# Optimization experiments

Measured on AMD Instinct MI355X. Metric: run time of the kernel, lower is better.

The kernel has to match this reference:

```python
import jax, jax.numpy as jnp
import numpy as np

N, E = 50000, 300000
IN_C, HID, OUT_C, HEADS = 256, 64, 128, 4
HW = HID * HEADS  # 256


def gat_conv(x, edge_index, W, att_src, att_dst, bias, concat):
    # x: [N, F_in], W: [F_in, H*C], att_*: [H, C], edge_index: [2, E] (src -> dst)
    H, C = att_src.shape
    n = x.shape[0]
    src, dst = edge_index[0], edge_index[1]
    h = (x @ W).reshape(n, H, C)                      # [N, H, C]
    a_src = jnp.einsum('nhc,hc->nh', h, att_src)      # [N, H]
    a_dst = jnp.einsum('nhc,hc->nh', h, att_dst)      # [N, H]
    e = jax.nn.leaky_relu(a_src[src] + a_dst[dst], 0.2)  # [E, H]
    m = jax.ops.segment_max(e, dst, num_segments=n)   # per-dst max for stable softmax
    m = jnp.where(jnp.isfinite(m), m, 0.0)
    ex = jnp.exp(e - m[dst])                          # [E, H]
    denom = jax.ops.segment_sum(ex, dst, num_segments=n)
    alpha = ex / (denom[dst] + 1e-16)                 # [E, H]
    msg = h[src] * alpha[:, :, None]                  # [E, H, C]
    out = jax.ops.segment_sum(msg, dst, num_segments=n)  # [N, H, C]
    if concat:
        return out.reshape(n, H * C) + bias
    return out.mean(axis=1) + bias


def setup_inputs() -> dict:
    key = jax.random.key(0)
    ks = jax.random.split(key, 24)
    inp = {}
    inp['x'] = jax.random.normal(ks[0], (N, IN_C), dtype=jnp.float32)
    inp['edge_index'] = jax.random.randint(ks[1], (2, E), 0, N, dtype=jnp.int32)
    def glorot(k, shape):
        fan = shape[0] + shape[-1]
        return jax.random.uniform(k, shape, jnp.float32, -1.0, 1.0) * np.sqrt(6.0 / fan)
    # layer 0: GATConv(256 -> 64, heads=4, concat) + Linear(256 -> 256)
    inp['W0'] = glorot(ks[2], (IN_C, HW)); inp['as0'] = glorot(ks[3], (HEADS, HID)); inp['ad0'] = glorot(ks[4], (HEADS, HID)); inp['b0'] = jnp.zeros((HW,), jnp.float32)
    inp['lw0'] = glorot(ks[5], (IN_C, HW)); inp['lb0'] = jnp.zeros((HW,), jnp.float32)
    # layer 1: GATConv(256 -> 64, heads=4, concat) + Linear(256 -> 256)
    inp['W1'] = glorot(ks[6], (HW, HW)); inp['as1'] = glorot(ks[7], (HEADS, HID)); inp['ad1'] = glorot(ks[8], (HEADS, HID)); inp['b1'] = jnp.zeros((HW,), jnp.float32)
    inp['lw1'] = glorot(ks[9], (HW, HW)); inp['lb1'] = jnp.zeros((HW,), jnp.float32)
    # layer 2: GATConv(256 -> 128, heads=4, concat=False mean) + Linear(256 -> 128)
    inp['W2'] = glorot(ks[10], (HW, HEADS * OUT_C)); inp['as2'] = glorot(ks[11], (HEADS, OUT_C)); inp['ad2'] = glorot(ks[12], (HEADS, OUT_C)); inp['b2'] = jnp.zeros((OUT_C,), jnp.float32)
    inp['lw2'] = glorot(ks[13], (HW, OUT_C)); inp['lb2'] = jnp.zeros((OUT_C,), jnp.float32)
    return inp


def reference(x, edge_index, W0, as0, ad0, b0, lw0, lb0, W1, as1, ad1, b1, lw1, lb1, W2, as2, ad2, b2, lw2, lb2):
    # layer 0
    h = gat_conv(x, edge_index, W0, as0, ad0, b0, concat=True) + (x @ lw0 + lb0)
    h = jax.nn.elu(h)  # dropout p=0.0 -> identity
    # layer 1
    h = gat_conv(h, edge_index, W1, as1, ad1, b1, concat=True) + (h @ lw1 + lb1)
    h = jax.nn.elu(h)
    # layer 2 (no activation)
    out = gat_conv(h, edge_index, W2, as2, ad2, b2, concat=False) + (h @ lw2 + lb2)
    return out
```

## Files before the change

### kernel.cpp

```cpp
#include <hip/hip_runtime.h>
#include <cstddef>


typedef __bf16 bf16x8 __attribute__((ext_vector_type(8)));
typedef float floatx4 __attribute__((ext_vector_type(4)));

__device__ __forceinline__ unsigned short bf16_rn(float f) {
    unsigned int u = __float_as_uint(f);
    u += 0x7FFF + ((u >> 16) & 1);
    return (unsigned short)(u >> 16);
}
__device__ __forceinline__ float bf16_tof(unsigned short h) {
    return __uint_as_float(((unsigned int)h) << 16);
}


__global__ void degree_kernel(const int* __restrict__ dst, int* __restrict__ deg, int E) {
    int e = blockIdx.x * 256 + threadIdx.x;
    if (e < E) atomicAdd(&deg[dst[e]], 1);
}

__global__ __launch_bounds__(1024) void scan_kernel(const int* __restrict__ deg,
                                                    int* __restrict__ off, int n) {
    __shared__ int wsum[16];
    __shared__ int carry_s;
    int tid = threadIdx.x, lane = tid & 63, wid = tid >> 6;
    if (tid == 0) { carry_s = 0; off[0] = 0; }
    __syncthreads();
    for (int base = 0; base < n; base += 1024) {
        int i = base + tid;
        int v = (i < n) ? deg[i] : 0;
        int s = v;
        #pragma unroll
        for (int d = 1; d < 64; d <<= 1) {
            int t = __shfl_up(s, d, 64);
            if (lane >= d) s += t;
        }
        if (lane == 63) wsum[wid] = s;
        __syncthreads();
        if (wid == 0) {
            int wv = (lane < 16) ? wsum[lane] : 0;
            #pragma unroll
            for (int d = 1; d < 16; d <<= 1) {
                int t = __shfl_up(wv, d, 64);
                if (lane >= d) wv += t;
            }
            if (lane < 16) wsum[lane] = wv;
        }
        __syncthreads();
        int prev = (wid > 0) ? wsum[wid - 1] : 0;
        int inc = carry_s + prev + s;
        if (i < n) off[i + 1] = inc;
        int chunk_total = wsum[15];
        __syncthreads();
        if (tid == 0) carry_s += chunk_total;
        __syncthreads();
    }
}

__global__ void scatter_kernel(const int* __restrict__ src, const int* __restrict__ dst,
                               const int* __restrict__ off, int* __restrict__ cursor,
                               int* __restrict__ csrc, int E) {
    int e = blockIdx.x * 256 + threadIdx.x;
    if (e < E) {
        int d = dst[e];
        int p = off[d] + atomicAdd(&cursor[d], 1);
        csrc[p] = src[e];
    }
}


__global__ __launch_bounds__(256) void wprep_kernel(
    const float* __restrict__ W0, const float* __restrict__ lw0,
    const float* __restrict__ W1, const float* __restrict__ lw1,
    const float* __restrict__ W2, const float* __restrict__ lw2,
    ushort* __restrict__ B0h, ushort* __restrict__ B0l,
    ushort* __restrict__ B1h, ushort* __restrict__ B1l,
    ushort* __restrict__ B2h, ushort* __restrict__ B2l,
    const float* __restrict__ as0, const float* __restrict__ ad0,
    const float* __restrict__ as1, const float* __restrict__ ad1,
    const float* __restrict__ as2, const float* __restrict__ ad2,
    float* __restrict__ vsd0, float* __restrict__ vsd1, float* __restrict__ vsd2)
{
    int bid = blockIdx.x, tid = threadIdx.x;
    if (bid < 1664) {
        const float* src; ushort* dh; ushort* dl; int Ncols, roff, base;
        if (bid < 256)       { src = W0;  dh = B0h; dl = B0l; Ncols = 256; roff = 0;   base = 0; }
        else if (bid < 512)  { src = lw0; dh = B0h; dl = B0l; Ncols = 256; roff = 256; base = 256; }
        else if (bid < 768)  { src = W1;  dh = B1h; dl = B1l; Ncols = 256; roff = 0;   base = 512; }
        else if (bid < 1024) { src = lw1; dh = B1h; dl = B1l; Ncols = 256; roff = 256; base = 768; }
        else if (bid < 1536) { src = W2;  dh = B2h; dl = B2l; Ncols = 512; roff = 0;   base = 1024; }
        else                 { src = lw2; dh = B2h; dl = B2l; Ncols = 128; roff = 512; base = 1536; }
        int idx = (bid - base) * 256 + tid;
        int k = idx / Ncols, n = idx - k * Ncols;
        float v = src[idx];
        unsigned short hi = bf16_rn(v);
        unsigned short lo = bf16_rn(v - bf16_tof(hi));
        int row = n + roff;
        int poff = ((row >> 4) * 8 + (k >> 5)) * 512 + (((row & 15) + 16 * ((k & 31) >> 3)) << 3) + (k & 7);
        dh[poff] = hi;
        dl[poff] = lo;
    } else {
        int fj = (bid - 1664) >> 2;
        int idx = ((bid - 1664) & 3) * 256 + tid;
        const float *W, *as_, *ad_; float* vsd; int C;
        if (fj == 0)      { W = W0; as_ = as0; ad_ = ad0; vsd = vsd0; C = 64; }
        else if (fj == 1) { W = W1; as_ = as1; ad_ = ad1; vsd = vsd1; C = 64; }
        else              { W = W2; as_ = as2; ad_ = ad2; vsd = vsd2; C = 128; }
        int k = idx >> 2, hh = idx & 3;
        const float* wp = W + (size_t)k * (4 * C) + hh * C;
        float s = 0.f, d = 0.f;
        for (int c = 0; c < C; c++) {
            float w = wp[c];
            s += w * as_[hh * C + c];
            d += w * ad_[hh * C + c];
        }
        vsd[k * 8 + hh] = s;
        vsd[k * 8 + 4 + hh] = d;
    }
}


__global__ __launch_bounds__(256) void split_att_kernel(
    const float* __restrict__ x, const float* __restrict__ vsd,
    ushort* __restrict__ Aph, ushort* __restrict__ Apl,
    float* __restrict__ asrc, float* __restrict__ adst, int n)
{
    int wid = threadIdx.x >> 6, lane = threadIdx.x & 63;
    int d = blockIdx.x * 4 + wid;
    if (d >= n) return;
    int k0 = lane * 4;
    float4 v = *(const float4*)(x + (size_t)d * 256 + k0);
    ushort4 hi, lo;
    hi.x = bf16_rn(v.x); lo.x = bf16_rn(v.x - bf16_tof(hi.x));
    hi.y = bf16_rn(v.y); lo.y = bf16_rn(v.y - bf16_tof(hi.y));
    hi.z = bf16_rn(v.z); lo.z = bf16_rn(v.z - bf16_tof(hi.z));
    hi.w = bf16_rn(v.w); lo.w = bf16_rn(v.w - bf16_tof(hi.w));
    int poff = ((d >> 4) * 8 + (k0 >> 5)) * 512 + (((d & 15) + 16 * ((k0 & 31) >> 3)) << 3) + (k0 & 7);
    *(ushort4*)(Aph + poff) = hi;
    *(ushort4*)(Apl + poff) = lo;

    const float* vp = vsd + (size_t)k0 * 8;
    float4 r0a = *(const float4*)(vp + 0),  r0b = *(const float4*)(vp + 4);
    float4 r1a = *(const float4*)(vp + 8),  r1b = *(const float4*)(vp + 12);
    float4 r2a = *(const float4*)(vp + 16), r2b = *(const float4*)(vp + 20);
    float4 r3a = *(const float4*)(vp + 24), r3b = *(const float4*)(vp + 28);
    float4 pa, pb;
    pa.x = v.x * r0a.x + v.y * r1a.x + v.z * r2a.x + v.w * r3a.x;
    pa.y = v.x * r0a.y + v.y * r1a.y + v.z * r2a.y + v.w * r3a.y;
    pa.z = v.x * r0a.z + v.y * r1a.z + v.z * r2a.z + v.w * r3a.z;
    pa.w = v.x * r0a.w + v.y * r1a.w + v.z * r2a.w + v.w * r3a.w;
    pb.x = v.x * r0b.x + v.y * r1b.x + v.z * r2b.x + v.w * r3b.x;
    pb.y = v.x * r0b.y + v.y * r1b.y + v.z * r2b.y + v.w * r3b.y;
    pb.z = v.x * r0b.z + v.y * r1b.z + v.z * r2b.z + v.w * r3b.z;
    pb.w = v.x * r0b.w + v.y * r1b.w + v.z * r2b.w + v.w * r3b.w;
    #pragma unroll
    for (int o = 1; o < 64; o <<= 1) {
        pa.x += __shfl_xor(pa.x, o, 64); pa.y += __shfl_xor(pa.y, o, 64);
        pa.z += __shfl_xor(pa.z, o, 64); pa.w += __shfl_xor(pa.w, o, 64);
        pb.x += __shfl_xor(pb.x, o, 64); pb.y += __shfl_xor(pb.y, o, 64);
        pb.z += __shfl_xor(pb.z, o, 64); pb.w += __shfl_xor(pb.w, o, 64);
    }
    if (lane == 0) {
        *(float4*)(asrc + (size_t)d * 4) = pa;
        *(float4*)(adst + (size_t)d * 4) = pb;
    }
}

__global__ __launch_bounds__(256) void amax_kernel(const float* __restrict__ asrc,
                                                   unsigned int* __restrict__ amax, int n) {
    int tid = threadIdx.x;
    float4 m4 = make_float4(-1e30f, -1e30f, -1e30f, -1e30f);
    for (int i = blockIdx.x * 256 + tid; i < n; i += gridDim.x * 256) {
        float4 v = ((const float4*)asrc)[i];
        m4.x = fmaxf(m4.x, v.x); m4.y = fmaxf(m4.y, v.y);
        m4.z = fmaxf(m4.z, v.z); m4.w = fmaxf(m4.w, v.w);
    }
    #pragma unroll
    for (int o = 32; o > 0; o >>= 1) {
        m4.x = fmaxf(m4.x, __shfl_down(m4.x, o, 64));
        m4.y = fmaxf(m4.y, __shfl_down(m4.y, o, 64));
        m4.z = fmaxf(m4.z, __shfl_down(m4.z, o, 64));
        m4.w = fmaxf(m4.w, __shfl_down(m4.w, o, 64));
    }
    __shared__ float sm[4][4];
    int wid = tid >> 6, lane = tid & 63;
    if (lane == 0) { sm[wid][0] = m4.x; sm[wid][1] = m4.y; sm[wid][2] = m4.z; sm[wid][3] = m4.w; }
    __syncthreads();
    if (tid < 4) {
        float v = fmaxf(fmaxf(sm[0][tid], sm[1][tid]), fmaxf(sm[2][tid], sm[3][tid]));
        unsigned int u = __float_as_uint(v);
        u = (u >> 31) ? ~u : (u | 0x80000000u);
        atomicMax(&amax[tid], u);
    }
}

__device__ __forceinline__ float amax_decode(unsigned int u) {
    unsigned int bits = (u >> 31) ? (u & 0x7FFFFFFFu) : ~u;
    return __uint_as_float(bits);
}


__global__ __launch_bounds__(256, 2) void gemm_mfma_kernel(
    const ushort* __restrict__ Aph, const ushort* __restrict__ Apl,
    const ushort* __restrict__ Bph, const ushort* __restrict__ Bpl,
    ushort* __restrict__ O1, int n1, ushort* __restrict__ O2,
    const float* __restrict__ bias2,
    int gm, int M, int N)
{
    int gy = N >> 7;
    int bid = blockIdx.x;
    int k8 = bid & 7, sb = bid >> 3;
    int ny = sb % gy, bxi = sb / gy;
    int bx = bxi * 8 + k8;
    if (bx >= gm) return;
    int bm = bx * 128, bn = ny * 128;

    int tid = threadIdx.x, lane = tid & 63, wv = tid >> 6;
    int wm = (wv >> 1) * 64, wn = (wv & 1) * 64;
    int fr = lane & 15, q = lane >> 4;

    size_t aoff = (size_t)((bm + wm) >> 4) * 4096 + lane * 8;
    size_t boff = (size_t)((bn + wn) >> 4) * 4096 + lane * 8;

    floatx4 acc[4][4] = {};
    bf16x8 cah[4], cal[4], cbh[4], cbl[4];
    bf16x8 nah[4], nal[4], nbh[4], nbl[4];

    #pragma unroll
    for (int i = 0; i < 4; ++i) {
        cah[i] = *(const bf16x8*)(Aph + aoff + i * 4096);
        cal[i] = *(const bf16x8*)(Apl + aoff + i * 4096);
        cbh[i] = *(const bf16x8*)(Bph + boff + i * 4096);
        cbl[i] = *(const bf16x8*)(Bpl + boff + i * 4096);
    }

    #pragma unroll
    for (int it = 0; it < 8; ++it) {
        if (it < 7) {
            int co = (it + 1) * 512;
            #pragma unroll
            for (int i = 0; i < 4; ++i) {
                nah[i] = *(const bf16x8*)(Aph + aoff + i * 4096 + co);
                nal[i] = *(const bf16x8*)(Apl + aoff + i * 4096 + co);
                nbh[i] = *(const bf16x8*)(Bph + boff + i * 4096 + co);
                nbl[i] = *(const bf16x8*)(Bpl + boff + i * 4096 + co);
            }
        }
        #pragma unroll
        for (int i = 0; i < 4; ++i)
            #pragma unroll
            for (int j = 0; j < 4; ++j) {
                acc[i][j] = __builtin_amdgcn_mfma_f32_16x16x32_bf16(cah[i], cbh[j], acc[i][j], 0, 0, 0);
                acc[i][j] = __builtin_amdgcn_mfma_f32_16x16x32_bf16(cah[i], cbl[j], acc[i][j], 0, 0, 0);
                acc[i][j] = __builtin_amdgcn_mfma_f32_16x16x32_bf16(cal[i], cbh[j], acc[i][j], 0, 0, 0);
            }
        if (it < 7) {
            #pragma unroll
            for (int i = 0; i < 4; ++i) {
                cah[i] = nah[i]; cal[i] = nal[i];
                cbh[i] = nbh[i]; cbl[i] = nbl[i];
            }
        }
    }

    int n2 = N - n1;
    #pragma unroll
    for (int i = 0; i < 4; ++i) {
        #pragma unroll
        for (int r = 0; r < 4; ++r) {
            int grow = bm + wm + i * 16 + q * 4 + r;
            if (grow < M) {
                #pragma unroll
                for (int j = 0; j < 4; ++j) {
                    int gcol = bn + wn + j * 16 + fr;
                    float v = acc[i][j][r];
                    if (gcol < n1) {
                        O1[(size_t)grow * n1 + gcol] = bf16_rn(v);
                    } else {
                        v += bias2[gcol - n1];
                        O2[(size_t)grow * n2 + (gcol - n1)] = bf16_rn(v);
                    }
                }
            }
        }
    }
}


__global__ __launch_bounds__(256, 8) void agg01_kernel(
    const ushort* __restrict__ h,
    const float* __restrict__ asrc, const float* __restrict__ adst,
    const unsigned int* __restrict__ amax,
    const int* __restrict__ off, const int* __restrict__ csrc,
    const ushort* __restrict__ lin,
    const float* __restrict__ bias,
    ushort* __restrict__ Aph, ushort* __restrict__ Apl,
    const float* __restrict__ vsd_next,
    float* __restrict__ asrc_out, float* __restrict__ adst_out,
    int n)
{
    int wid = threadIdx.x >> 6, lane = threadIdx.x & 63;
    int d = blockIdx.x * 4 + wid;
    if (d >= n) return;
    int head = lane >> 4;
    int c0 = lane * 4;
    float a_d = adst[d * 4 + head];
    float mh = amax_decode(amax[head]) + a_d;
    float m = (mh > 0.f) ? mh : 0.2f * mh;
    int s0 = off[d], s1 = off[d + 1];

    float denom = 0.f, a0 = 0.f, a1 = 0.f, a2 = 0.f, a3 = 0.f;
    int i = s0;
    for (; i + 4 <= s1; i += 4) {
        int sa = csrc[i], sb = csrc[i + 1], sc = csrc[i + 2], sd = csrc[i + 3];
        float ea = asrc[sa * 4 + head];
        float eb = asrc[sb * 4 + head];
        float ec = asrc[sc * 4 + head];
        float ed = asrc[sd * 4 + head];
        ushort4 hva = *(const ushort4*)(h + (size_t)sa * 256 + c0);
        ushort4 hvb = *(const ushort4*)(h + (size_t)sb * 256 + c0);
        ushort4 hvc = *(const ushort4*)(h + (size_t)sc * 256 + c0);
        ushort4 hvd = *(const ushort4*)(h + (size_t)sd * 256 + c0);
        ea += a_d; ea = (ea > 0.f) ? ea : 0.2f * ea; float wa = __expf(ea - m);
        eb += a_d; eb = (eb > 0.f) ? eb : 0.2f * eb; float wb = __expf(eb - m);
        ec += a_d; ec = (ec > 0.f) ? ec : 0.2f * ec; float wc = __expf(ec - m);
        ed += a_d; ed = (ed > 0.f) ? ed : 0.2f * ed; float wd = __expf(ed - m);
        denom += wa;
        a0 += wa * bf16_tof(hva.x); a1 += wa * bf16_tof(hva.y);
        a2 += wa * bf16_tof(hva.z); a3 += wa * bf16_tof(hva.w);
        denom += wb;
        a0 += wb * bf16_tof(hvb.x); a1 += wb * bf16_tof(hvb.y);
        a2 += wb * bf16_tof(hvb.z); a3 += wb * bf16_tof(hvb.w);
        denom += wc;
        a0 += wc * bf16_tof(hvc.x); a1 += wc * bf16_tof(hvc.y);
        a2 += wc * bf16_tof(hvc.z); a3 += wc * bf16_tof(hvc.w);
        denom += wd;
        a0 += wd * bf16_tof(hvd.x); a1 += wd * bf16_tof(hvd.y);
        a2 += wd * bf16_tof(hvd.z); a3 += wd * bf16_tof(hvd.w);
    }
    for (; i < s1; ++i) {
        int s = csrc[i];
        float e = asrc[s * 4 + head] + a_d;
        e = (e > 0.f) ? e : 0.2f * e;
        float w = __expf(e - m);
        denom += w;
        ushort4 hv = *(const ushort4*)(h + (size_t)s * 256 + c0);
        a0 += w * bf16_tof(hv.x);
        a1 += w * bf16_tof(hv.y);
        a2 += w * bf16_tof(hv.z);
        a3 += w * bf16_tof(hv.w);
    }
    float inv = 1.f / (denom + 1e-16f);
    float4 b4 = *(const float4*)(bias + c0);
    ushort4 l4 = *(const ushort4*)(lin + (size_t)d * 256 + c0);
    float v0 = a0 * inv + b4.x + bf16_tof(l4.x);
    float v1 = a1 * inv + b4.y + bf16_tof(l4.y);
    float v2 = a2 * inv + b4.z + bf16_tof(l4.z);
    float v3 = a3 * inv + b4.w + bf16_tof(l4.w);
    v0 = (v0 > 0.f) ? v0 : (__expf(v0) - 1.f);
    v1 = (v1 > 0.f) ? v1 : (__expf(v1) - 1.f);
    v2 = (v2 > 0.f) ? v2 : (__expf(v2) - 1.f);
    v3 = (v3 > 0.f) ? v3 : (__expf(v3) - 1.f);

    ushort4 oh, ol;
    oh.x = bf16_rn(v0); ol.x = bf16_rn(v0 - bf16_tof(oh.x));
    oh.y = bf16_rn(v1); ol.y = bf16_rn(v1 - bf16_tof(oh.y));
    oh.z = bf16_rn(v2); ol.z = bf16_rn(v2 - bf16_tof(oh.z));
    oh.w = bf16_rn(v3); ol.w = bf16_rn(v3 - bf16_tof(oh.w));
    int poff = ((d >> 4) * 8 + (c0 >> 5)) * 512 + (((d & 15) + 16 * ((c0 & 31) >> 3)) << 3) + (c0 & 7);
    *(ushort4*)(Aph + poff) = oh;
    *(ushort4*)(Apl + poff) = ol;

    const float* vp = vsd_next + (size_t)c0 * 8;
    float4 r0a = *(const float4*)(vp + 0),  r0b = *(const float4*)(vp + 4);
    float4 r1a = *(const float4*)(vp + 8),  r1b = *(const float4*)(vp + 12);
    float4 r2a = *(const float4*)(vp + 16), r2b = *(const float4*)(vp + 20);
    float4 r3a = *(const float4*)(vp + 24), r3b = *(const float4*)(vp + 28);
    float4 pa, pb;
    pa.x = v0 * r0a.x + v1 * r1a.x + v2 * r2a.x + v3 * r3a.x;
    pa.y = v0 * r0a.y + v1 * r1a.y + v2 * r2a.y + v3 * r3a.y;
    pa.z = v0 * r0a.z + v1 * r1a.z + v2 * r2a.z + v3 * r3a.z;
    pa.w = v0 * r0a.w + v1 * r1a.w + v2 * r2a.w + v3 * r3a.w;
    pb.x = v0 * r0b.x + v1 * r1b.x + v2 * r2b.x + v3 * r3b.x;
    pb.y = v0 * r0b.y + v1 * r1b.y + v2 * r2b.y + v3 * r3b.y;
    pb.z = v0 * r0b.z + v1 * r1b.z + v2 * r2b.z + v3 * r3b.z;
    pb.w = v0 * r0b.w + v1 * r1b.w + v2 * r2b.w + v3 * r3b.w;
    #pragma unroll
    for (int o = 1; o < 64; o <<= 1) {
        pa.x += __shfl_xor(pa.x, o, 64); pa.y += __shfl_xor(pa.y, o, 64);
        pa.z += __shfl_xor(pa.z, o, 64); pa.w += __shfl_xor(pa.w, o, 64);
        pb.x += __shfl_xor(pb.x, o, 64); pb.y += __shfl_xor(pb.y, o, 64);
        pb.z += __shfl_xor(pb.z, o, 64); pb.w += __shfl_xor(pb.w, o, 64);
    }
    if (lane == 0) {
        *(float4*)(asrc_out + (size_t)d * 4) = pa;
        *(float4*)(adst_out + (size_t)d * 4) = pb;
    }
}


__global__ __launch_bounds__(256, 8) void agg2_kernel(
    const ushort* __restrict__ h,
    const float* __restrict__ asrc, const float* __restrict__ adst,
    const unsigned int* __restrict__ amax,
    const int* __restrict__ off, const int* __restrict__ csrc,
    const ushort* __restrict__ lin,
    const float* __restrict__ bias,
    float* __restrict__ out,
    int n)
{
    int wid = threadIdx.x >> 6, lane = threadIdx.x & 63;
    int d = blockIdx.x * 4 + wid;
    if (d >= n) return;
    int ha = lane >> 5;
    int hb = ha + 2;
    int c0 = lane * 4;
    float ad_a = adst[d * 4 + ha];
    float ad_b = adst[d * 4 + hb];
    float mha = amax_decode(amax[ha]) + ad_a;
    float mhb = amax_decode(amax[hb]) + ad_b;
    float ma = (mha > 0.f) ? mha : 0.2f * mha;
    float mb = (mhb > 0.f) ? mhb : 0.2f * mhb;
    int s0 = off[d], s1 = off[d + 1];

    float da = 0.f, db = 0.f;
    floatx4 aa = {0.f, 0.f, 0.f, 0.f}, ab = {0.f, 0.f, 0.f, 0.f};
    int i = s0;
    for (; i + 2 <= s1; i += 2) {
        int sx = csrc[i], sy = csrc[i + 1];
        float eax = asrc[sx * 4 + ha];
        float ebx = asrc[sx * 4 + hb];
        float eay = asrc[sy * 4 + ha];
        float eby = asrc[sy * 4 + hb];
        ushort4 vax = *(const ushort4*)(h + (size_t)sx * 512 + c0);
        ushort4 vbx = *(const ushort4*)(h + (size_t)sx * 512 + 256 + c0);
        ushort4 vay = *(const ushort4*)(h + (size_t)sy * 512 + c0);
        ushort4 vby = *(const ushort4*)(h + (size_t)sy * 512 + 256 + c0);
        eax += ad_a; eax = (eax > 0.f) ? eax : 0.2f * eax; float wax = __expf(eax - ma);
        ebx += ad_b; ebx = (ebx > 0.f) ? ebx : 0.2f * ebx; float wbx = __expf(ebx - mb);
        eay += ad_a; eay = (eay > 0.f) ? eay : 0.2f * eay; float way = __expf(eay - ma);
        eby += ad_b; eby = (eby > 0.f) ? eby : 0.2f * eby; float wby = __expf(eby - mb);
        da += wax; db += wbx;
        aa[0] += wax * bf16_tof(vax.x); aa[1] += wax * bf16_tof(vax.y);
        aa[2] += wax * bf16_tof(vax.z); aa[3] += wax * bf16_tof(vax.w);
        ab[0] += wbx * bf16_tof(vbx.x); ab[1] += wbx * bf16_tof(vbx.y);
        ab[2] += wbx * bf16_tof(vbx.z); ab[3] += wbx * bf16_tof(vbx.w);
        da += way; db += wby;
        aa[0] += way * bf16_tof(vay.x); aa[1] += way * bf16_tof(vay.y);
        aa[2] += way * bf16_tof(vay.z); aa[3] += way * bf16_tof(vay.w);
        ab[0] += wby * bf16_tof(vby.x); ab[1] += wby * bf16_tof(vby.y);
        ab[2] += wby * bf16_tof(vby.z); ab[3] += wby * bf16_tof(vby.w);
    }
    for (; i < s1; ++i) {
        int s = csrc[i];
        float ea = asrc[s * 4 + ha] + ad_a;
        float eb = asrc[s * 4 + hb] + ad_b;
        ea = (ea > 0.f) ? ea : 0.2f * ea;
        eb = (eb > 0.f) ? eb : 0.2f * eb;
        float wa = __expf(ea - ma), wb = __expf(eb - mb);
        da += wa; db += wb;
        ushort4 va = *(const ushort4*)(h + (size_t)s * 512 + c0);
        ushort4 vb = *(const ushort4*)(h + (size_t)s * 512 + 256 + c0);
        aa[0] += wa * bf16_tof(va.x); aa[1] += wa * bf16_tof(va.y);
        aa[2] += wa * bf16_tof(va.z); aa[3] += wa * bf16_tof(va.w);
        ab[0] += wb * bf16_tof(vb.x); ab[1] += wb * bf16_tof(vb.y);
        ab[2] += wb * bf16_tof(vb.z); ab[3] += wb * bf16_tof(vb.w);
    }
    float ia = 1.f / (da + 1e-16f), ib = 1.f / (db + 1e-16f);
    float s4[4];
    #pragma unroll
    for (int j = 0; j < 4; ++j) s4[j] = aa[j] * ia + ab[j] * ib;
    float p4[4];
    #pragma unroll
    for (int j = 0; j < 4; ++j) p4[j] = __shfl_xor(s4[j], 32, 64);
    if (lane < 32) {
        float4 b4 = *(const float4*)(bias + c0);
        ushort4 l4 = *(const ushort4*)(lin + (size_t)d * 128 + c0);
        float4 o;
        o.x = 0.25f * (s4[0] + p4[0]) + b4.x + bf16_tof(l4.x);
        o.y = 0.25f * (s4[1] + p4[1]) + b4.y + bf16_tof(l4.y);
        o.z = 0.25f * (s4[2] + p4[2]) + b4.z + bf16_tof(l4.z);
        o.w = 0.25f * (s4[3] + p4[3]) + b4.w + bf16_tof(l4.w);
        *(float4*)(out + (size_t)d * 128 + c0) = o;
    }
}


extern "C" void kernel_launch(void* const* d_in, const int* in_sizes, int n_in,
                              void* d_out, int out_size, void* d_ws, size_t ws_size,
                              hipStream_t stream)
{
    const float* x   = (const float*)d_in[0];
    const int*   ei  = (const int*)d_in[1];
    const float* W0  = (const float*)d_in[2];
    const float* as0 = (const float*)d_in[3];
    const float* ad0 = (const float*)d_in[4];
    const float* b0  = (const float*)d_in[5];
    const float* lw0 = (const float*)d_in[6];
    const float* lb0 = (const float*)d_in[7];
    const float* W1  = (const float*)d_in[8];
    const float* as1 = (const float*)d_in[9];
    const float* ad1 = (const float*)d_in[10];
    const float* b1  = (const float*)d_in[11];
    const float* lw1 = (const float*)d_in[12];
    const float* lb1 = (const float*)d_in[13];
    const float* W2  = (const float*)d_in[14];
    const float* as2 = (const float*)d_in[15];
    const float* ad2 = (const float*)d_in[16];
    const float* b2  = (const float*)d_in[17];
    const float* lw2 = (const float*)d_in[18];
    const float* lb2 = (const float*)d_in[19];
    float* out = (float*)d_out;

    const int N = in_sizes[0] / 256;
    const int E = in_sizes[1] / 2;
    const int* esrc = ei;
    const int* edst = ei + E;

    const int gm = (N + 127) / 128;
    const int gmp = ((gm + 7) / 8) * 8;
    const size_t Agroups = (size_t)gm * 8;

    char* p = (char*)d_ws;
    ushort* act_hi = (ushort*)p; p += Agroups * 8 * 512 * 2;
    ushort* act_lo = (ushort*)p; p += Agroups * 8 * 512 * 2;
    ushort* h      = (ushort*)p; p += (size_t)N * 512 * 2;
    ushort* lin    = (ushort*)p; p += (size_t)N * 256 * 2;
    float*  as_a   = (float*)p;  p += (size_t)N * 4 * 4;
    float*  ad_a   = (float*)p;  p += (size_t)N * 4 * 4;
    float*  as_b   = (float*)p;  p += (size_t)N * 4 * 4;
    float*  ad_b   = (float*)p;  p += (size_t)N * 4 * 4;
    ushort* B0h = (ushort*)p; p += (size_t)32 * 8 * 512 * 2;
    ushort* B0l = (ushort*)p; p += (size_t)32 * 8 * 512 * 2;
    ushort* B1h = (ushort*)p; p += (size_t)32 * 8 * 512 * 2;
    ushort* B1l = (ushort*)p; p += (size_t)32 * 8 * 512 * 2;
    ushort* B2h = (ushort*)p; p += (size_t)40 * 8 * 512 * 2;
    ushort* B2l = (ushort*)p; p += (size_t)40 * 8 * 512 * 2;
    float* vsd0 = (float*)p; p += 256 * 8 * 4;
    float* vsd1 = (float*)p; p += 256 * 8 * 4;
    float* vsd2 = (float*)p; p += 256 * 8 * 4;
    unsigned int* amax = (unsigned int*)p;
    int* deg    = (int*)(amax + 12);
    int* off    = deg + N;
    int* cursor = off + N + 1;
    int* csrc   = cursor + N;

    hipMemsetAsync(amax, 0, sizeof(int) * (size_t)(3 * N + 13), stream);

    int egrid = (E + 255) / 256;
    degree_kernel<<<egrid, 256, 0, stream>>>(edst, deg, E);
    scan_kernel<<<1, 1024, 0, stream>>>(deg, off, N);
    scatter_kernel<<<egrid, 256, 0, stream>>>(esrc, edst, off, cursor, csrc, E);

    wprep_kernel<<<1676, 256, 0, stream>>>(W0, lw0, W1, lw1, W2, lw2,
                                           B0h, B0l, B1h, B1l, B2h, B2l,
                                           as0, ad0, as1, ad1, as2, ad2,
                                           vsd0, vsd1, vsd2);

    int g4 = (N + 3) / 4;

    split_att_kernel<<<g4, 256, 0, stream>>>(x, vsd0, act_hi, act_lo, as_a, ad_a, N);
    amax_kernel<<<32, 256, 0, stream>>>(as_a, amax + 0, N);

    gemm_mfma_kernel<<<gmp * 4, 256, 0, stream>>>(act_hi, act_lo, B0h, B0l, h, 256, lin, lb0, gm, N, 512);
    agg01_kernel<<<g4, 256, 0, stream>>>(h, as_a, ad_a, amax + 0, off, csrc, lin, b0,
                                         act_hi, act_lo, vsd1, as_b, ad_b, N);
    amax_kernel<<<32, 256, 0, stream>>>(as_b, amax + 4, N);

    gemm_mfma_kernel<<<gmp * 4, 256, 0, stream>>>(act_hi, act_lo, B1h, B1l, h, 256, lin, lb1, gm, N, 512);
    agg01_kernel<<<g4, 256, 0, stream>>>(h, as_b, ad_b, amax + 4, off, csrc, lin, b1,
                                         act_hi, act_lo, vsd2, as_a, ad_a, N);
    amax_kernel<<<32, 256, 0, stream>>>(as_a, amax + 8, N);

    gemm_mfma_kernel<<<gmp * 5, 256, 0, stream>>>(act_hi, act_lo, B2h, B2l, h, 512, lin, lb2, gm, N, 640);
    agg2_kernel<<<g4, 256, 0, stream>>>(h, as_a, ad_a, amax + 8, off, csrc, lin, b2, out, N);
}
```

Before: 752.1 us.

## Stage GEMM A tiles through LDS with direct global-to-LDS loads, double-buffered

The A operand (hi/lo bf16 split) of the MFMA GEMM is now loaded cooperatively into double-buffered shared memory with global_load_lds, rather than each wave loading its own copy from global memory into registers. This removes the duplicated A loads between the two waves that share a row tile and cuts the register prefetch buffers. Occupancy is raised to 3 blocks per SM. B is still read directly per iteration without prefetch, and a block-wide barrier is added every K step, which may expose B load latency.

New measurement: 697.2 us. 7.3% less time.

```diff
diff --git a/kernel.cpp b/kernel.cpp
--- a/kernel.cpp
+++ b/kernel.cpp
@@ -12,6 +12,12 @@
 }
 __device__ __forceinline__ float bf16_tof(unsigned short h) {
     return __uint_as_float(((unsigned int)h) << 16);
+}
+
+__device__ __forceinline__ void gload_lds16(const void* g, void* l) {
+    __builtin_amdgcn_global_load_lds(
+        (const __attribute__((address_space(1))) unsigned int*)g,
+        (__attribute__((address_space(3))) unsigned int*)l, 16, 0, 0);
 }
 
 
@@ -201,13 +207,14 @@
 }
 
 
-__global__ __launch_bounds__(256, 2) void gemm_mfma_kernel(
+__global__ __launch_bounds__(256, 3) void gemm_mfma_kernel(
     const ushort* __restrict__ Aph, const ushort* __restrict__ Apl,
     const ushort* __restrict__ Bph, const ushort* __restrict__ Bpl,
     ushort* __restrict__ O1, int n1, ushort* __restrict__ O2,
     const float* __restrict__ bias2,
     int gm, int M, int N)
 {
+    __shared__ __align__(16) char smem[32768];
     int gy = N >> 7;
     int bid = blockIdx.x;
     int k8 = bid & 7, sb = bid >> 3;
@@ -220,32 +227,41 @@
     int wm = (wv >> 1) * 64, wn = (wv & 1) * 64;
     int fr = lane & 15, q = lane >> 4;
 
-    size_t aoff = (size_t)((bm + wm) >> 4) * 4096 + lane * 8;
-    size_t boff = (size_t)((bn + wn) >> 4) * 4096 + lane * 8;
+    const ushort* sp = (wv < 2) ? Aph : Apl;
+    size_t gsrc = ((size_t)(bm >> 4) + (size_t)((wv & 1) * 4)) * 4096 + (size_t)lane * 8;
+    int lreg = ((wv >> 1) * 8192) + ((wv & 1) * 4096);
+
+    size_t boff = (size_t)((bn + wn) >> 4) * 4096 + (size_t)lane * 8;
+    int agl = (wv >> 1) * 4;
 
     floatx4 acc[4][4] = {};
-    bf16x8 cah[4], cal[4], cbh[4], cbl[4];
-    bf16x8 nah[4], nal[4], nbh[4], nbl[4];
-
-    #pragma unroll
-    for (int i = 0; i < 4; ++i) {
-        cah[i] = *(const bf16x8*)(Aph + aoff + i * 4096);
-        cal[i] = *(const bf16x8*)(Apl + aoff + i * 4096);
-        cbh[i] = *(const bf16x8*)(Bph + boff + i * 4096);
-        cbl[i] = *(const bf16x8*)(Bpl + boff + i * 4096);
-    }
+
+    #pragma unroll
+    for (int t = 0; t < 4; ++t)
+        gload_lds16(sp + gsrc + (size_t)t * 4096, smem + lreg + t * 1024);
+    __syncthreads();
 
     #pragma unroll
     for (int it = 0; it < 8; ++it) {
+        int cur = (it & 1) << 14;
+        bf16x8 cbh[4], cbl[4];
+        #pragma unroll
+        for (int j = 0; j < 4; ++j) {
+            cbh[j] = *(const bf16x8*)(Bph + boff + j * 4096 + it * 512);
+            cbl[j] = *(const bf16x8*)(Bpl + boff + j * 4096 + it * 512);
+        }
         if (it < 7) {
-            int co = (it + 1) * 512;
+            int nb = ((it + 1) & 1) << 14;
+            size_t co = gsrc + (size_t)(it + 1) * 512;
             #pragma unroll
-            for (int i = 0; i < 4; ++i) {
-                nah[i] = *(const bf16x8*)(Aph + aoff + i * 4096 + co);
-                nal[i] = *(const bf16x8*)(Apl + aoff + i * 4096 + co);
-                nbh[i] = *(const bf16x8*)(Bph + boff + i * 4096 + co);
-                nbl[i] = *(const bf16x8*)(Bpl + boff + i * 4096 + co);
-            }
+            for (int t = 0; t < 4; ++t)
+                gload_lds16(sp + co + (size_t)t * 4096, smem + nb + lreg + t * 1024);
+        }
+        bf16x8 cah[4], cal[4];
+        #pragma unroll
+        for (int i = 0; i < 4; ++i) {
+            cah[i] = *(const bf16x8*)(smem + cur + (agl + i) * 1024 + lane * 16);
+            cal[i] = *(const bf16x8*)(smem + cur + 8192 + (agl + i) * 1024 + lane * 16);
         }
         #pragma unroll
         for (int i = 0; i < 4; ++i)
@@ -255,13 +271,7 @@
                 acc[i][j] = __builtin_amdgcn_mfma_f32_16x16x32_bf16(cah[i], cbl[j], acc[i][j], 0, 0, 0);
                 acc[i][j] = __builtin_amdgcn_mfma_f32_16x16x32_bf16(cal[i], cbh[j], acc[i][j], 0, 0, 0);
             }
-        if (it < 7) {
-            #pragma unroll
-            for (int i = 0; i < 4; ++i) {
-                cah[i] = nah[i]; cal[i] = nal[i];
-                cbh[i] = nbh[i]; cbl[i] = nbl[i];
-            }
-        }
+        if (it < 7) __syncthreads();
     }
 
     int n2 = N - n1;
```
